# Performance work log

Hardware: AMD Instinct MI355X
Metric: run time of the kernel (lower is better)

The kernel has to match this reference:

```python
import jax, jax.numpy as jnp
import numpy as np

DIM, HEADS = 1024, 16
B, N = 2, 2048


def setup_inputs() -> dict:
    key = jax.random.key(0)
    ks = jax.random.split(key, 8)
    d = DIM // HEADS
    return {
        "x": jax.random.normal(ks[0], (B, N, DIM), dtype=jnp.float32),
        "w_qkv": jax.random.normal(ks[1], (DIM, 3 * DIM), dtype=jnp.float32) * (DIM ** -0.5),
        "w_out": jax.random.normal(ks[2], (DIM, DIM), dtype=jnp.float32) * (DIM ** -0.5),
        "b_out": jnp.zeros((DIM,), dtype=jnp.float32),
        "void_q": jax.random.normal(ks[3], (1, HEADS, 1, d), dtype=jnp.float32),
        "void_k": jax.random.normal(ks[4], (1, HEADS, 1, d), dtype=jnp.float32),
        "void_v": jax.random.normal(ks[5], (1, HEADS, 1, d), dtype=jnp.float32),
        "attention_trace": jax.random.uniform(ks[6], (HEADS, 1, 1), dtype=jnp.float32),
        "temperature_factor": jax.random.normal(ks[7], (HEADS, 1, 1), dtype=jnp.float32),
    }


def reference(x, w_qkv, w_out, b_out, void_q, void_k, void_v,
              attention_trace, temperature_factor):
    b, n, dim = x.shape
    h = void_q.shape[1]
    d = dim // h

    qkv = x @ w_qkv  # [b, n, 3*dim]
    q, k, v = jnp.split(qkv, 3, axis=-1)

    def to_heads(t):
        return t.reshape(b, n, h, d).transpose(0, 2, 1, 3)  # b h n d

    q, k, v = to_heads(q), to_heads(k), to_heads(v)

    # append the void token to q, k, v -> seq length n+1
    q = jnp.concatenate([q, jnp.broadcast_to(void_q, (b, h, 1, d))], axis=2)
    k = jnp.concatenate([k, jnp.broadcast_to(void_k, (b, h, 1, d))], axis=2)
    v = jnp.concatenate([v, jnp.broadcast_to(void_v, (b, h, 1, d))], axis=2)

    # NOTE: original scales by full dim**-0.5, not head-dim
    dots = jnp.einsum('bhid,bhjd->bhij', q, k) * (dim ** -0.5)
    # void-to-void bias of +10 at index [n, n]
    dots = dots.at[:, :, n, n].add(10.0)

    # stateful per-head temperature (trace is a buffer, treated as input)
    temperature = jnp.maximum(1.0 + jnp.abs(attention_trace) * temperature_factor, 1.0)  # [h,1,1]
    attn = jax.nn.softmax(dots / temperature, axis=-1)  # [b, h, n+1, n+1]

    out = jnp.einsum('bhij,bhjd->bhid', attn, v)[:, :, :n, :]  # drop void row
    out = out.transpose(0, 2, 1, 3).reshape(b, n, dim)  # b n (h d)
    return out @ w_out + b_out
```

## Files before the change

### kernel.cpp

```cpp
#include <hip/hip_runtime.h>
#include <stdint.h>

#define DIMF   1024
#define HEADS  16
#define HD     64
#define BB     2
#define NN     2048
#define NKP    2112
#define NTILE  33

typedef __attribute__((ext_vector_type(8))) __bf16 bf16x8;
typedef __attribute__((ext_vector_type(4))) float  f32x4;

__device__ __forceinline__ float b2f(uint16_t h) {
  union { uint32_t u; float f; } v; v.u = ((uint32_t)h) << 16; return v.f;
}
__device__ __forceinline__ uint16_t f2b(float f) {
  union { float f; uint32_t u; } v; v.f = f;
  uint32_t r = v.u + 0x7FFFu + ((v.u >> 16) & 1u);
  return (uint16_t)(r >> 16);
}

__device__ __forceinline__ void gl_lds16(const void* g, void* l) {
  __builtin_amdgcn_global_load_lds(
      (const __attribute__((address_space(1))) void*)g,
      (__attribute__((address_space(3))) void*)l, 16, 0, 0);
}

__global__ __launch_bounds__(256) void cvt_f32_bf16(const float* __restrict__ src,
                                                    uint16_t* __restrict__ dst, int n4) {
  int i = blockIdx.x * 256 + threadIdx.x;
  if (i < n4) {
    float4 v = *(const float4*)&src[i * 4];
    uint16_t* d = dst + i * 4;
    d[0] = f2b(v.x); d[1] = f2b(v.y); d[2] = f2b(v.z); d[3] = f2b(v.w);
  }
}

__global__ __launch_bounds__(256) void transpose_k(const float* __restrict__ src,
                                                   uint16_t* __restrict__ dst, int M, int N) {
  __shared__ uint16_t tile[32][33];
  int bx = blockIdx.x * 32, by = blockIdx.y * 32;
  int x = threadIdx.x, y0 = threadIdx.y;
#pragma unroll
  for (int i = 0; i < 32; i += 8)
    tile[y0 + i][x] = f2b(src[(size_t)(by + y0 + i) * N + bx + x]);
  __syncthreads();
#pragma unroll
  for (int i = 0; i < 32; i += 8)
    dst[(size_t)(bx + y0 + i) * M + by + x] = tile[x][y0 + i];
}

__global__ __launch_bounds__(256) void fill_void(const float* __restrict__ vk,
                                                 const float* __restrict__ vv,
                                                 uint16_t* __restrict__ k_ws,
                                                 uint16_t* __restrict__ vt_ws) {
  int idx = blockIdx.x * 256 + threadIdx.x;
  int dd = idx & 63;
  int r  = (idx >> 6) & 63;
  int bh = idx >> 12;
  int h  = bh & (HEADS - 1);
  uint16_t kv  = (r == 0) ? f2b(vk[h * HD + dd]) : (uint16_t)0;
  uint16_t vvv = (r == 0) ? f2b(vv[h * HD + dd]) : (uint16_t)0;
  k_ws[((size_t)bh * NKP + NN + r) * HD + dd]  = kv;
  vt_ws[((size_t)bh * HD + dd) * NKP + NN + r] = vvv;
}

template<int EPI>
__global__ __launch_bounds__(256) void gemm_bt(const uint16_t* __restrict__ A,
                                               const uint16_t* __restrict__ Bt,
                                               int K, int Nout,
                                               uint16_t* __restrict__ o0,
                                               uint16_t* __restrict__ o1,
                                               uint16_t* __restrict__ o2,
                                               float* __restrict__ fo,
                                               const float* __restrict__ bias) {
  __shared__ uint16_t lds_a[128][32];
  __shared__ uint16_t lds_b[128][32];
  const int m0 = blockIdx.y * 128, n0 = blockIdx.x * 128;
  const int tid = threadIdx.x, lane = tid & 63, wid = tid >> 6;
  const int wm = (wid >> 1) * 64, wn = (wid & 1) * 64;
  const int lr = lane & 15, lg = lane >> 4;
  f32x4 acc[4][4] = {};
  for (int k0 = 0; k0 < K; k0 += 32) {
    __syncthreads();
#pragma unroll
    for (int it = 0; it < 2; ++it) {
      const int chunk = wid * 2 + it;
      const int o = chunk * 1024 + lane * 16;
      const int r = o >> 6, cb = o & 63;
      gl_lds16((const char*)&A[(size_t)(m0 + r) * K + k0] + cb,
               (char*)&lds_a[0][0] + chunk * 1024);
      gl_lds16((const char*)&Bt[(size_t)(n0 + r) * K + k0] + cb,
               (char*)&lds_b[0][0] + chunk * 1024);
    }
    __syncthreads();
    bf16x8 af[4], bf[4];
#pragma unroll
    for (int i = 0; i < 4; ++i)
      af[i] = *(const bf16x8*)((const char*)&lds_a[0][0] + (wm + i * 16 + lr) * 64 + lg * 16);
#pragma unroll
    for (int j = 0; j < 4; ++j)
      bf[j] = *(const bf16x8*)((const char*)&lds_b[0][0] + (wn + j * 16 + lr) * 64 + lg * 16);
#pragma unroll
    for (int i = 0; i < 4; ++i)
#pragma unroll
      for (int j = 0; j < 4; ++j)
        acc[i][j] = __builtin_amdgcn_mfma_f32_16x16x32_bf16(af[i], bf[j], acc[i][j], 0, 0, 0);
  }
#pragma unroll
  for (int i = 0; i < 4; ++i)
#pragma unroll
    for (int j = 0; j < 4; ++j)
#pragma unroll
      for (int r = 0; r < 4; ++r) {
        int mg = m0 + wm + i * 16 + lg * 4 + r;
        int ng = n0 + wn + j * 16 + lr;
        float v = acc[i][j][r];
        if (EPI == 0) {
          int b = mg >> 11, n = mg & (NN - 1);
          int which = ng >> 10, rem = ng & (DIMF - 1), h = rem >> 6, dd = rem & 63;
          int bh = b * HEADS + h;
          uint16_t bv = f2b(v);
          if (which == 0)      o0[((size_t)bh * NN + n) * HD + dd] = bv;
          else if (which == 1) o1[((size_t)bh * NKP + n) * HD + dd] = bv;
          else                 o2[((size_t)bh * HD + dd) * NKP + n] = bv;
        } else {
          fo[(size_t)mg * Nout + ng] = v + bias[ng];
        }
      }
}

__global__ __launch_bounds__(256) void attn_k(const uint16_t* __restrict__ q_ws,
                                              const uint16_t* __restrict__ k_ws,
                                              const uint16_t* __restrict__ vt_ws,
                                              const float* __restrict__ trace,
                                              const float* __restrict__ factor,
                                              uint16_t* __restrict__ o_ws) {
  __shared__ uint16_t ldsk[64][64];
  __shared__ uint16_t ldsv[64][64];
  __shared__ uint16_t ldsp[4][16][72];
  const int bh = blockIdx.x;
  const int qb = blockIdx.y;
  const int h = bh & (HEADS - 1), b = bh >> 4;
  const int tid = threadIdx.x, lane = tid & 63, wid = tid >> 6;
  const int lr = lane & 15, lg = lane >> 4;

  const float temp  = fmaxf(1.0f + fabsf(trace[h]) * factor[h], 1.0f);
  const float scale = 0.03125f / temp;

  const int qrow0 = qb * 64 + wid * 16;
  const uint16_t* qrow = q_ws + ((size_t)bh * NN + qrow0 + lr) * HD;
  bf16x8 qf[2];
  qf[0] = *(const bf16x8*)(qrow + lg * 8);
  qf[1] = *(const bf16x8*)(qrow + 32 + lg * 8);

  f32x4 acc[4] = {};
  float lsum[4] = {0.f, 0.f, 0.f, 0.f};

  for (int t = 0; t < NTILE; ++t) {
    const int t0 = t * 64;
    __syncthreads();
#pragma unroll
    for (int it = 0; it < 2; ++it) {
      const int chunk = wid * 2 + it;
      const int o = chunk * 1024 + lane * 16;
      const int r = o >> 7, cb = o & 127;
      const int scb = cb ^ ((r & 7) << 4);
      gl_lds16((const char*)&k_ws[((size_t)bh * NKP + t0 + r) * HD] + scb,
               (char*)&ldsk[0][0] + chunk * 1024);
      gl_lds16((const char*)&vt_ws[((size_t)bh * HD + r) * NKP + t0] + scb,
               (char*)&ldsv[0][0] + chunk * 1024);
    }
    __syncthreads();

    f32x4 s[4];
#pragma unroll
    for (int c = 0; c < 4; ++c) {
      f32x4 sa = {};
#pragma unroll
      for (int kk = 0; kk < 2; ++kk) {
        const int row = c * 16 + lr;
        const int cbb = (kk * 64 + lg * 16) ^ ((row & 7) << 4);
        bf16x8 kf = *(const bf16x8*)((const char*)&ldsk[0][0] + row * 128 + cbb);
        sa = __builtin_amdgcn_mfma_f32_16x16x32_bf16(qf[kk], kf, sa, 0, 0, 0);
      }
      s[c] = sa;
    }
#pragma unroll
    for (int c = 0; c < 4; ++c)
#pragma unroll
      for (int r = 0; r < 4; ++r) {
        float p = __expf(s[c][r] * scale);
        lsum[r] += p;
        ldsp[wid][lg * 4 + r][c * 16 + lr] = f2b(p);
      }
    asm volatile("" ::: "memory");
    __builtin_amdgcn_sched_barrier(0);
#pragma unroll
    for (int kk = 0; kk < 2; ++kk) {
      bf16x8 pf = *(const bf16x8*)&ldsp[wid][lr][kk * 32 + lg * 8];
#pragma unroll
      for (int cd = 0; cd < 4; ++cd) {
        const int row = cd * 16 + lr;
        const int cbb = (kk * 64 + lg * 16) ^ ((row & 7) << 4);
        bf16x8 vf = *(const bf16x8*)((const char*)&ldsv[0][0] + row * 128 + cbb);
        acc[cd] = __builtin_amdgcn_mfma_f32_16x16x32_bf16(pf, vf, acc[cd], 0, 0, 0);
      }
    }
  }
#pragma unroll
  for (int r = 0; r < 4; ++r) {
    float l = lsum[r];
    l += __shfl_xor(l, 1); l += __shfl_xor(l, 2);
    l += __shfl_xor(l, 4); l += __shfl_xor(l, 8);
    l -= 63.0f;
    const float inv = 1.0f / l;
    const int n = qrow0 + lg * 4 + r;
    size_t base = ((size_t)b * NN + n) * DIMF + h * HD;
#pragma unroll
    for (int cd = 0; cd < 4; ++cd)
      o_ws[base + cd * 16 + lr] = f2b(acc[cd][r] * inv);
  }
}

extern "C" void kernel_launch(void* const* d_in, const int* in_sizes, int n_in,
                              void* d_out, int out_size, void* d_ws, size_t ws_size,
                              hipStream_t stream) {
  const float* x      = (const float*)d_in[0];
  const float* wqkv   = (const float*)d_in[1];
  const float* wout   = (const float*)d_in[2];
  const float* bout   = (const float*)d_in[3];
  const float* voidk  = (const float*)d_in[5];
  const float* voidv  = (const float*)d_in[6];
  const float* trace  = (const float*)d_in[7];
  const float* factor = (const float*)d_in[8];
  float* out = (float*)d_out;

  uint16_t* ws    = (uint16_t*)d_ws;
  uint16_t* x_bf  = ws;
  uint16_t* o_ws  = x_bf;
  uint16_t* wqkvT = x_bf  + 4194304;
  uint16_t* woutT = wqkvT + 3145728;
  uint16_t* q_ws  = woutT + 1048576;
  uint16_t* k_ws  = q_ws  + 4194304;
  uint16_t* vt_ws = k_ws  + 4325376;

  cvt_f32_bf16<<<dim3(4194304 / 4 / 256), dim3(256), 0, stream>>>(x, x_bf, 4194304 / 4);
  transpose_k<<<dim3(3072 / 32, 1024 / 32), dim3(32, 8), 0, stream>>>(wqkv, wqkvT, 1024, 3072);
  transpose_k<<<dim3(1024 / 32, 1024 / 32), dim3(32, 8), 0, stream>>>(wout, woutT, 1024, 1024);
  fill_void<<<dim3(512), dim3(256), 0, stream>>>(voidk, voidv, k_ws, vt_ws);
  gemm_bt<0><<<dim3(3072 / 128, 4096 / 128), dim3(256), 0, stream>>>(
      x_bf, wqkvT, 1024, 3072, q_ws, k_ws, vt_ws, nullptr, nullptr);
  attn_k<<<dim3(HEADS * BB, NN / 64), dim3(256), 0, stream>>>(
      q_ws, k_ws, vt_ws, trace, factor, o_ws);
  gemm_bt<1><<<dim3(1024 / 128, 4096 / 128), dim3(256), 0, stream>>>(
      o_ws, woutT, 1024, 1024, nullptr, nullptr, nullptr, out, bout);
}
```

Before: 161.2 us.

## Merge prep kernels, hoist LDS addresses, add setprio and truncating bf16 in attention

Merges four preprocessing launches into two: the x conversion with the void fill, and both weight transposes into one grid using blockIdx.z. In the attention kernel, the swizzled LDS address computation moves out of the tile loop, and s_setprio brackets the MFMA sections. The f2b rounding of softmax probabilities becomes truncation, with the row sum built from the same truncated value so numerator and denominator stay consistent. This trims launch overhead and per-tile ALU work, at the cost of a slight change in probability rounding.

```diff
diff --git a/kernel.cpp b/kernel.cpp
--- a/kernel.cpp
+++ b/kernel.cpp
@@ -27,43 +27,49 @@
       (__attribute__((address_space(3))) void*)l, 16, 0, 0);
 }
 
-__global__ __launch_bounds__(256) void cvt_f32_bf16(const float* __restrict__ src,
-                                                    uint16_t* __restrict__ dst, int n4) {
-  int i = blockIdx.x * 256 + threadIdx.x;
-  if (i < n4) {
-    float4 v = *(const float4*)&src[i * 4];
-    uint16_t* d = dst + i * 4;
+__global__ __launch_bounds__(256) void prep_k(const float* __restrict__ x,
+                                              uint16_t* __restrict__ x_bf,
+                                              const float* __restrict__ vk,
+                                              const float* __restrict__ vv,
+                                              uint16_t* __restrict__ k_ws,
+                                              uint16_t* __restrict__ vt_ws) {
+  if (blockIdx.x < 4096) {
+    int i = blockIdx.x * 256 + threadIdx.x;
+    float4 v = *(const float4*)&x[(size_t)i * 4];
+    uint16_t* d = x_bf + (size_t)i * 4;
     d[0] = f2b(v.x); d[1] = f2b(v.y); d[2] = f2b(v.z); d[3] = f2b(v.w);
-  }
-}
-
-__global__ __launch_bounds__(256) void transpose_k(const float* __restrict__ src,
-                                                   uint16_t* __restrict__ dst, int M, int N) {
+  } else {
+    int idx = (blockIdx.x - 4096) * 256 + threadIdx.x;
+    int dd = idx & 63;
+    int r  = (idx >> 6) & 63;
+    int bh = idx >> 12;
+    int h  = bh & (HEADS - 1);
+    uint16_t kv  = (r == 0) ? f2b(vk[h * HD + dd]) : (uint16_t)0;
+    uint16_t vvv = (r == 0) ? f2b(vv[h * HD + dd]) : (uint16_t)0;
+    k_ws[((size_t)bh * NKP + NN + r) * HD + dd]  = kv;
+    vt_ws[((size_t)bh * HD + dd) * NKP + NN + r] = vvv;
+  }
+}
+
+__global__ __launch_bounds__(256) void transpose2_k(const float* __restrict__ w1,
+                                                    uint16_t* __restrict__ d1,
+                                                    const float* __restrict__ w2,
+                                                    uint16_t* __restrict__ d2) {
+  const int z = blockIdx.z;
+  if (z == 1 && blockIdx.x >= 32) return;
+  const float* src = z ? w2 : w1;
+  uint16_t*   dst = z ? d2 : d1;
+  const int M = 1024, N = z ? 1024 : 3072;
   __shared__ uint16_t tile[32][33];
   int bx = blockIdx.x * 32, by = blockIdx.y * 32;
-  int x = threadIdx.x, y0 = threadIdx.y;
-#pragma unroll
-  for (int i = 0; i < 32; i += 8)
+  int x = threadIdx.x & 31, y0 = (threadIdx.x >> 5) * 4;
+#pragma unroll
+  for (int i = 0; i < 4; ++i)
     tile[y0 + i][x] = f2b(src[(size_t)(by + y0 + i) * N + bx + x]);
   __syncthreads();
 #pragma unroll
-  for (int i = 0; i < 32; i += 8)
+  for (int i = 0; i < 4; ++i)
     dst[(size_t)(bx + y0 + i) * M + by + x] = tile[x][y0 + i];
-}
-
-__global__ __launch_bounds__(256) void fill_void(const float* __restrict__ vk,
-                                                 const float* __restrict__ vv,
-                                                 uint16_t* __restrict__ k_ws,
-                                                 uint16_t* __restrict__ vt_ws) {
-  int idx = blockIdx.x * 256 + threadIdx.x;
-  int dd = idx & 63;
-  int r  = (idx >> 6) & 63;
-  int bh = idx >> 12;
-  int h  = bh & (HEADS - 1);
-  uint16_t kv  = (r == 0) ? f2b(vk[h * HD + dd]) : (uint16_t)0;
-  uint16_t vvv = (r == 0) ? f2b(vv[h * HD + dd]) : (uint16_t)0;
-  k_ws[((size_t)bh * NKP + NN + r) * HD + dd]  = kv;
-  vt_ws[((size_t)bh * HD + dd) * NKP + NN + r] = vvv;
 }
 
 template<int EPI>
@@ -155,6 +161,13 @@
   qf[0] = *(const bf16x8*)(qrow + lg * 8);
   qf[1] = *(const bf16x8*)(qrow + 32 + lg * 8);
 
+  const int rsw = (lr & 7) << 4;
+  const char* kb0 = (const char*)&ldsk[0][0] + lr * 128 + ((lg * 16) ^ rsw);
+  const char* kb1 = (const char*)&ldsk[0][0] + lr * 128 + ((64 + lg * 16) ^ rsw);
+  const char* vb0 = (const char*)&ldsv[0][0] + lr * 128 + ((lg * 16) ^ rsw);
+  const char* vb1 = (const char*)&ldsv[0][0] + lr * 128 + ((64 + lg * 16) ^ rsw);
+  const char* pr  = (const char*)&ldsp[wid][lr][lg * 8];
+
   f32x4 acc[4] = {};
   float lsum[4] = {0.f, 0.f, 0.f, 0.f};
 
@@ -177,37 +190,38 @@
     f32x4 s[4];
 #pragma unroll
     for (int c = 0; c < 4; ++c) {
+      bf16x8 kf0 = *(const bf16x8*)(kb0 + c * 2048);
+      bf16x8 kf1 = *(const bf16x8*)(kb1 + c * 2048);
       f32x4 sa = {};
-#pragma unroll
-      for (int kk = 0; kk < 2; ++kk) {
-        const int row = c * 16 + lr;
-        const int cbb = (kk * 64 + lg * 16) ^ ((row & 7) << 4);
-        bf16x8 kf = *(const bf16x8*)((const char*)&ldsk[0][0] + row * 128 + cbb);
-        sa = __builtin_amdgcn_mfma_f32_16x16x32_bf16(qf[kk], kf, sa, 0, 0, 0);
-      }
+      __builtin_amdgcn_s_setprio(1);
+      sa = __builtin_amdgcn_mfma_f32_16x16x32_bf16(qf[0], kf0, sa, 0, 0, 0);
+      sa = __builtin_amdgcn_mfma_f32_16x16x32_bf16(qf[1], kf1, sa, 0, 0, 0);
+      __builtin_amdgcn_s_setprio(0);
       s[c] = sa;
     }
 #pragma unroll
     for (int c = 0; c < 4; ++c)
 #pragma unroll
       for (int r = 0; r < 4; ++r) {
-        float p = __expf(s[c][r] * scale);
-        lsum[r] += p;
-        ldsp[wid][lg * 4 + r][c * 16 + lr] = f2b(p);
+        union { float f; uint32_t u; } pv;
+        pv.f = __expf(s[c][r] * scale);
+        ldsp[wid][lg * 4 + r][c * 16 + lr] = (uint16_t)(pv.u >> 16);
+        pv.u &= 0xffff0000u;
+        lsum[r] += pv.f;
       }
     asm volatile("" ::: "memory");
     __builtin_amdgcn_sched_barrier(0);
+    __builtin_amdgcn_s_setprio(1);
 #pragma unroll
     for (int kk = 0; kk < 2; ++kk) {
-      bf16x8 pf = *(const bf16x8*)&ldsp[wid][lr][kk * 32 + lg * 8];
+      bf16x8 pf = *(const bf16x8*)(pr + kk * 64);
 #pragma unroll
       for (int cd = 0; cd < 4; ++cd) {
-        const int row = cd * 16 + lr;
-        const int cbb = (kk * 64 + lg * 16) ^ ((row & 7) << 4);
-        bf16x8 vf = *(const bf16x8*)((const char*)&ldsv[0][0] + row * 128 + cbb);
+        bf16x8 vf = *(const bf16x8*)((kk ? vb1 : vb0) + cd * 2048);
         acc[cd] = __builtin_amdgcn_mfma_f32_16x16x32_bf16(pf, vf, acc[cd], 0, 0, 0);
       }
     }
+    __builtin_amdgcn_s_setprio(0);
   }
 #pragma unroll
   for (int r = 0; r < 4; ++r) {
@@ -246,10 +260,8 @@
   uint16_t* k_ws  = q_ws  + 4194304;
   uint16_t* vt_ws = k_ws  + 4325376;
 
-  cvt_f32_bf16<<<dim3(4194304 / 4 / 256), dim3(256), 0, stream>>>(x, x_bf, 4194304 / 4);
-  transpose_k<<<dim3(3072 / 32, 1024 / 32), dim3(32, 8), 0, stream>>>(wqkv, wqkvT, 1024, 3072);
-  transpose_k<<<dim3(1024 / 32, 1024 / 32), dim3(32, 8), 0, stream>>>(wout, woutT, 1024, 1024);
-  fill_void<<<dim3(512), dim3(256), 0, stream>>>(voidk, voidv, k_ws, vt_ws);
+  prep_k<<<dim3(4608), dim3(256), 0, stream>>>(x, x_bf, voidk, voidv, k_ws, vt_ws);
+  transpose2_k<<<dim3(96, 32, 2), dim3(256), 0, stream>>>(wqkv, wqkvT, wout, woutT);
   gemm_bt<0><<<dim3(3072 / 128, 4096 / 128), dim3(256), 0, stream>>>(
       x_bf, wqkvT, 1024, 3072, q_ws, k_ws, vt_ws, nullptr, nullptr);
   attn_k<<<dim3(HEADS * BB, NN / 64), dim3(256), 0, stream>>>(
```

Measured after the change: 154.1 us. 1.05x faster.
